# Kernel tuning notes

Hardware: AMD Instinct MI355X
Metric: run time of the kernel (lower is better)

Reference implementation:

```python
import jax, jax.numpy as jnp
import numpy as np

B, C1, H, W = 8, 256, 192, 192
P = 4              # effective patch size (even, <= H,W)
ROUTE_RATIO = 0.25
MIN_REGIONS = 1
HIDDEN = 128       # max(int(c1*0.5), 16)
ROUTE_HIDDEN = 64  # max(HIDDEN//2, 16)
EPS = 1e-5


def conv2d(x, w, groups=1, pad=0):
    return jax.lax.conv_general_dilated(
        x, w, (1, 1), [(pad, pad), (pad, pad)],
        dimension_numbers=("NCHW", "OIHW", "NCHW"),
        feature_group_count=groups)


def bn(x, g, b):
    # eval-mode BatchNorm with running_mean=0, running_var=1
    scale = g / jnp.sqrt(1.0 + EPS)
    return x * scale[None, :, None, None] + b[None, :, None, None]


def pixel_unshuffle(x, r):
    n, c, h, w = x.shape
    x = x.reshape(n, c, h // r, r, w // r, r)
    return x.transpose(0, 1, 3, 5, 2, 4).reshape(n, c * r * r, h // r, w // r)


def pixel_shuffle(x, r):
    n, cr, h, w = x.shape
    c = cr // (r * r)
    x = x.reshape(n, c, r, r, h, w)
    return x.transpose(0, 1, 4, 2, 5, 3).reshape(n, c, h * r, w * r)


def setup_inputs() -> dict:
    key = jax.random.key(0)
    ks = jax.random.split(key, 8)
    c4 = C1 * 4
    inp = {
        "x": jax.random.normal(ks[0], (B, C1, H, W), jnp.float32),
        # route head: 1x1 conv (no bias) -> BN -> SiLU -> 1x1 conv (bias)
        "rw1": jax.random.normal(ks[1], (ROUTE_HIDDEN, C1, 1, 1), jnp.float32) / np.sqrt(C1),
        "rg1": jnp.ones((ROUTE_HIDDEN,), jnp.float32),
        "rb1": jnp.zeros((ROUTE_HIDDEN,), jnp.float32),
        "rw2": jax.random.normal(ks[2], (1, ROUTE_HIDDEN, 1, 1), jnp.float32) / np.sqrt(ROUTE_HIDDEN),
        "rbias2": jnp.zeros((1,), jnp.float32),
        # expert: Conv(4c->hidden,1x1)+BN+SiLU, DWConv(3x3)+BN+SiLU, Conv(hidden->4c,1x1)+BN
        "ew1": jax.random.normal(ks[3], (HIDDEN, c4, 1, 1), jnp.float32) / np.sqrt(c4),
        "eg1": jnp.ones((HIDDEN,), jnp.float32),
        "eb1": jnp.zeros((HIDDEN,), jnp.float32),
        "dww": jax.random.normal(ks[4], (HIDDEN, 1, 3, 3), jnp.float32) / 3.0,
        "dwg": jnp.ones((HIDDEN,), jnp.float32),
        "dwb": jnp.zeros((HIDDEN,), jnp.float32),
        "ew2": jax.random.normal(ks[5], (c4, HIDDEN, 1, 1), jnp.float32) / np.sqrt(HIDDEN),
        "eg2": jnp.ones((c4,), jnp.float32),
        "eb2": jnp.zeros((c4,), jnp.float32),
    }
    return inp


def reference(x, rw1, rg1, rb1, rw2, rbias2, ew1, eg1, eb1, dww, dwg, dwb, ew2, eg2, eb2):
    b, c, h, w = x.shape
    p = P
    pad_h = (p - h % p) % p
    pad_w = (p - w % p) % p
    x_pad = jnp.pad(x, ((0, 0), (0, 0), (0, pad_h), (0, pad_w)))
    hp, wp = h + pad_h, w + pad_w
    gh, gw = hp // p, wp // p
    num_patches = gh * gw
    k = min(num_patches, max(MIN_REGIONS, int(np.ceil(num_patches * ROUTE_RATIO))))

    # router: avg-pool each patch, 1x1 MLP -> per-patch score
    pooled = x_pad.reshape(b, c, gh, p, gw, p).mean(axis=(3, 5))          # [b,c,gh,gw]
    r1 = jax.nn.silu(bn(conv2d(pooled, rw1), rg1, rb1))
    logits = conv2d(r1, rw2) + rbias2[None, :, None, None]
    scores = jax.nn.sigmoid(logits).reshape(b, num_patches)               # [b,N]
    top_vals, top_idx = jax.lax.top_k(scores, k)                          # [b,k]

    # gather selected patches
    patches = x_pad.reshape(b, c, gh, p, gw, p).transpose(0, 2, 4, 1, 3, 5)
    patches = patches.reshape(b, num_patches, c, p, p)
    sel = jnp.take_along_axis(patches, top_idx[:, :, None, None, None], axis=1)
    sel = sel.reshape(b * k, c, p, p)

    # expert on pixel-unshuffled patches
    y = pixel_unshuffle(sel, 2)                                           # [bk, 4c, p/2, p/2]
    y = jax.nn.silu(bn(conv2d(y, ew1), eg1, eb1))
    y = jax.nn.silu(bn(conv2d(y, dww, groups=HIDDEN, pad=1), dwg, dwb))
    y = bn(conv2d(y, ew2), eg2, eb2)
    refined = pixel_shuffle(y, 2).reshape(b, k, c, p, p)
    refined = refined * top_vals[:, :, None, None, None]

    # scatter back into zero residual
    delta = jnp.zeros((b, num_patches, c, p, p), x.dtype)
    delta = delta.at[jnp.arange(b)[:, None], top_idx].set(refined)
    delta = delta.reshape(b, gh, gw, c, p, p).transpose(0, 3, 1, 4, 2, 5)
    delta = delta.reshape(b, c, hp, wp)
    return delta[..., :h, :w]
```

## Files before the change

### kernel.cpp

```cpp
#include <hip/hip_runtime.h>
#include <hip/hip_bf16.h>

typedef __attribute__((ext_vector_type(8))) short bf16x8;
typedef __attribute__((ext_vector_type(4))) float f32x4;

#define NB 8
#define C1 256
#define HH 192
#define WW 192
#define GH 48
#define GW 48
#define NP 2304
#define KSEL 576
#define RH 64
#define HID 128
#define C4 1024
#define HW (HH*WW)

#define WS_FLAG 0
#define WS_F 64
#define WS_W16 81280ull
#define WS_POOLED 605696ull
#define WS_PSCALE WS_POOLED
#define WS_SCORES 19480064ull

#define F_RW1 0
#define F_RG1 16384
#define F_RB1 16448
#define F_RW2 16512
#define F_RBIAS2 16576
#define F_EG1 16580
#define F_EB1 16708
#define F_DWW 16836
#define F_DWG 17988
#define F_DWB 18116
#define F_EG2 18244
#define F_EB2 19268

__device__ __forceinline__ float b2f(unsigned short h) {
  return __uint_as_float(((unsigned)h) << 16);
}
__device__ __forceinline__ unsigned short f2b(float f) {
  unsigned u = __float_as_uint(f);
  u += 0x7FFF + ((u >> 16) & 1u);
  return (unsigned short)(u >> 16);
}
__device__ __forceinline__ float siluf(float v) { return v / (1.f + expf(-v)); }

__global__ void k_detect(const unsigned short* xb, char* ws) {
  __shared__ int cnt[256];
  int t = threadIdx.x;
  int c = 0;
  for (int s = 0; s < 32; ++s) {
    unsigned short u = xb[(t * 32 + s) * 2];
    int e = (u >> 7) & 0xFF;
    c += (u == 0 || (e >= 90 && e <= 145)) ? 1 : 0;
  }
  cnt[t] = c;
  __syncthreads();
  for (int s = 128; s > 0; s >>= 1) {
    if (t < s) cnt[t] += cnt[t + s];
    __syncthreads();
  }
  if (t == 0) *(int*)(ws + WS_FLAG) = (cnt[0] >= 4915) ? 1 : 0;
}

__global__ void k_prep(const void* rw1, const void* rg1, const void* rb1, const void* rw2,
                       const void* rbias2, const void* ew1, const void* eg1, const void* eb1,
                       const void* dww, const void* dwg, const void* dwb, const void* ew2,
                       const void* eg2, const void* eb2, char* ws) {
  int bf = *(const int*)(ws + WS_FLAG);
  float* F = (float*)(ws + WS_F);
  unsigned short* W16 = (unsigned short*)(ws + WS_W16);
  int i = blockIdx.x * 256 + threadIdx.x;
  if (i >= 282433) return;
  if (i < 20289) {
    const void* src; int si; int dof;
    if      (i < 16384) { src = rw1;    si = i;          dof = F_RW1 + si; }
    else if (i < 16448) { src = rg1;    si = i - 16384;  dof = F_RG1 + si; }
    else if (i < 16512) { src = rb1;    si = i - 16448;  dof = F_RB1 + si; }
    else if (i < 16576) { src = rw2;    si = i - 16512;  dof = F_RW2 + si; }
    else if (i < 16577) { src = rbias2; si = i - 16576;  dof = F_RBIAS2 + si; }
    else if (i < 16705) { src = eg1;    si = i - 16577;  dof = F_EG1 + si; }
    else if (i < 16833) { src = eb1;    si = i - 16705;  dof = F_EB1 + si; }
    else if (i < 17985) { src = dww;    si = i - 16833;  dof = F_DWW + si; }
    else if (i < 18113) { src = dwg;    si = i - 17985;  dof = F_DWG + si; }
    else if (i < 18241) { src = dwb;    si = i - 18113;  dof = F_DWB + si; }
    else if (i < 19265) { src = eg2;    si = i - 18241;  dof = F_EG2 + si; }
    else                { src = eb2;    si = i - 19265;  dof = F_EB2 + si; }
    F[dof] = bf ? b2f(((const unsigned short*)src)[si]) : ((const float*)src)[si];
  } else {
    int j = i - 20289;
    const void* src; int si; int dof;
    if (j < 131072) { src = ew1; si = j;          dof = j; }
    else            { src = ew2; si = j - 131072; dof = j; }
    W16[dof] = bf ? ((const unsigned short*)src)[si]
                  : f2b(((const float*)src)[si]);
  }
}

template<int BF>
__global__ void k_pool(const void* xin, char* ws) {
  if ((*(const int*)(ws + WS_FLAG) != 0) != (BF != 0)) return;
  float* pooled = (float*)(ws + WS_POOLED);
  int tid = blockIdx.x * 256 + threadIdx.x;
  int px = tid % GW;
  int t2 = tid / GW;
  int py = t2 % GH;
  int bc = t2 / GH;
  size_t base = (size_t)bc * HW + (size_t)(py * 4) * WW + px * 4;
  float s = 0.f;
#pragma unroll
  for (int r = 0; r < 4; ++r) {
    if (BF) {
      const ushort4 v = *(const ushort4*)((const unsigned short*)xin + base + r * WW);
      s += b2f(v.x) + b2f(v.y) + b2f(v.z) + b2f(v.w);
    } else {
      const float4 v = *(const float4*)((const float*)xin + base + r * WW);
      s += v.x + v.y + v.z + v.w;
    }
  }
  pooled[tid] = s * 0.0625f;
}

__global__ __launch_bounds__(512, 2) void k_mlp(char* ws) {
  const float* F = (const float*)(ws + WS_F);
  const float* pooled = (const float*)(ws + WS_POOLED);
  float* scores = (float*)(ws + WS_SCORES);
  __shared__ float LP[256][68];
  __shared__ float LR[8 * 64];
  const int t = threadIdx.x;
  const int b = blockIdx.x / 36;
  const int pos0 = (blockIdx.x % 36) * 64;

  {
    const int pc = t & 15, c0 = t >> 4;
    const float* src = pooled + (size_t)(b * C1) * NP + pos0 + pc * 4;
#pragma unroll
    for (int s = 0; s < 8; ++s) {
      int c = c0 + 32 * s;
      float4 v = *(const float4*)(src + (size_t)c * NP);
      *(float4*)&LP[c][pc * 4] = v;
    }
  }
  __syncthreads();

  const int lane = t & 63;
  const int q = __builtin_amdgcn_readfirstlane(t >> 6);
  const float* wq = F + F_RW1 + q * 8 * C1;
  float acc[8];
#pragma unroll
  for (int j = 0; j < 8; ++j) acc[j] = 0.f;
  for (int c = 0; c < 256; c += 4) {
    float p0 = LP[c + 0][lane];
    float p1 = LP[c + 1][lane];
    float p2 = LP[c + 2][lane];
    float p3 = LP[c + 3][lane];
#pragma unroll
    for (int j = 0; j < 8; ++j) {
      acc[j] += wq[j * C1 + c + 0] * p0;
      acc[j] += wq[j * C1 + c + 1] * p1;
      acc[j] += wq[j * C1 + c + 2] * p2;
      acc[j] += wq[j * C1 + c + 3] * p3;
    }
  }
  const float BNS = 1.f / sqrtf(1.f + 1e-5f);
  float lp = 0.f;
#pragma unroll
  for (int j = 0; j < 8; ++j) {
    int h = q * 8 + j;
    float v = acc[j] * (F[F_RG1 + h] * BNS) + F[F_RB1 + h];
    lp += F[F_RW2 + h] * siluf(v);
  }
  LR[q * 64 + lane] = lp;
  __syncthreads();
  if (t < 64) {
    float s = F[F_RBIAS2];
#pragma unroll
    for (int j = 0; j < 8; ++j) s += LR[j * 64 + t];
    scores[b * NP + pos0 + t] = 1.f / (1.f + expf(-s));
  }
}

__global__ void k_route(char* ws) {
  const float* scores = (const float*)(ws + WS_SCORES);
  float* pscale = (float*)(ws + WS_PSCALE);
  int b = blockIdx.x / 9, r = blockIdx.x % 9;
  __shared__ float s[NP];
  for (int i = threadIdx.x; i < NP; i += 256) s[i] = scores[b * NP + i];
  __syncthreads();
  int i = r * 256 + threadIdx.x;
  float si = s[i];
  int rank = 0;
  for (int j = 0; j < NP; ++j) {
    float sj = s[j];
    rank += (sj > si || (sj == si && j < i)) ? 1 : 0;
  }
  pscale[b * NP + i] = (rank < KSEL) ? si : 0.f;
}


#define XLOAD(P_, cc_) do { \
    size_t o_ = (size_t)(cc_) * 16 * HW; \
    if (BF) { P_##h0 = *(const ushort4*)(xh + xoff0 + o_); \
              P_##h1 = *(const ushort4*)(xh + xoff1 + o_); } \
    else    { P_##f0 = *(const float4*)(xf + xoff0 + o_); \
              P_##f1 = *(const float4*)(xf + xoff1 + o_); } \
    const unsigned short* wp_ = W1b + (cc_) * 64; \
    P_##w0 = *(const uint4*)(wp_ + wi0); \
    P_##w1 = *(const uint4*)(wp_ + wi1); \
  } while(0)

#define XWRITE(P_, UT_, WC_) do { \
    unsigned lo0_, hi0_, lo1_, hi1_; \
    if (BF) { lo0_ = P_##h0.x | ((unsigned)P_##h0.y << 16); hi0_ = P_##h0.z | ((unsigned)P_##h0.w << 16); \
              lo1_ = P_##h1.x | ((unsigned)P_##h1.y << 16); hi1_ = P_##h1.z | ((unsigned)P_##h1.w << 16); } \
    else    { lo0_ = f2b(P_##f0.x) | ((unsigned)f2b(P_##f0.y) << 16); hi0_ = f2b(P_##f0.z) | ((unsigned)f2b(P_##f0.w) << 16); \
              lo1_ = f2b(P_##f1.x) | ((unsigned)f2b(P_##f1.y) << 16); hi1_ = f2b(P_##f1.z) | ((unsigned)f2b(P_##f1.w) << 16); } \
    *(unsigned*)&UT_[n_lo72 + kb0] = lo0_; \
    *(unsigned*)&UT_[n_hi72 + kb0] = hi0_; \
    *(unsigned*)&UT_[n_lo72 + kb1] = lo1_; \
    *(unsigned*)&UT_[n_hi72 + kb1] = hi1_; \
    *(uint4*)&WC_[wcw0] = P_##w0; \
    *(uint4*)&WC_[wcw1] = P_##w1; \
  } while(0)

#define MFMA1(WCO_, B_, ACC_) ACC_ = __builtin_amdgcn_mfma_f32_16x16x32_bf16(*(const bf16x8*)&WC_[wc_off + (WCO_)], B_, ACC_, 0, 0, 0)

#define G1_MFMA(UT_, WCp_) do { \
    const unsigned short* WC_ = WCp_; \
    bf16x8 b0_ = *(const bf16x8*)&UT_[ut_off]; \
    bf16x8 b1_ = *(const bf16x8*)&UT_[ut_off + 32]; \
    MFMA1(0, b0_, acc10);    MFMA1(1152, b0_, acc11); \
    MFMA1(2304, b0_, acc12); MFMA1(3456, b0_, acc13); \
    MFMA1(32, b1_, acc10);   MFMA1(1152+32, b1_, acc11); \
    MFMA1(2304+32, b1_, acc12); MFMA1(3456+32, b1_, acc13); \
  } while(0)

#define G1EPI(ACC_, mi_) do { \
    _Pragma("unroll") \
    for (int r_ = 0; r_ < 4; ++r_) { \
      int h_ = 64 * wm + 16 * (mi_) + l4 * 4 + r_; \
      O1[h_ * 68 + otc] = siluf(ACC_[r_] * (F[F_EG1 + h_] * BNS) + F[F_EB1 + h_]); \
    } \
  } while(0)

#define G2_STEP(P_, WCp_, mt_) do { \
    const unsigned short* WC_ = WCp_; \
    *(uint4*)&((unsigned short*)WCp_)[w2a] = P_##a; \
    *(uint4*)&((unsigned short*)WCp_)[w2b] = P_##b; \
    if ((mt_) < 14) { \
      const unsigned short* wp_ = W2b + (size_t)((mt_) + 2) * 8192; \
      P_##a = *(const uint4*)(wp_ + w2s); \
      P_##b = *(const uint4*)(wp_ + w2s + 64); \
    } \
    __syncthreads(); \
    f32x4 a20 = (f32x4){0.f, 0.f, 0.f, 0.f}; \
    f32x4 a21 = (f32x4){0.f, 0.f, 0.f, 0.f}; \
    a20 = __builtin_amdgcn_mfma_f32_16x16x32_bf16(*(const bf16x8*)&WC_[g2_off + 0],        bq0, a20, 0,0,0); \
    a21 = __builtin_amdgcn_mfma_f32_16x16x32_bf16(*(const bf16x8*)&WC_[g2_off + 2176],     bq0, a21, 0,0,0); \
    a20 = __builtin_amdgcn_mfma_f32_16x16x32_bf16(*(const bf16x8*)&WC_[g2_off + 32],       bq1, a20, 0,0,0); \
    a21 = __builtin_amdgcn_mfma_f32_16x16x32_bf16(*(const bf16x8*)&WC_[g2_off + 2176+32],  bq1, a21, 0,0,0); \
    a20 = __builtin_amdgcn_mfma_f32_16x16x32_bf16(*(const bf16x8*)&WC_[g2_off + 64],       bq2, a20, 0,0,0); \
    a21 = __builtin_amdgcn_mfma_f32_16x16x32_bf16(*(const bf16x8*)&WC_[g2_off + 2176+64],  bq2, a21, 0,0,0); \
    a20 = __builtin_amdgcn_mfma_f32_16x16x32_bf16(*(const bf16x8*)&WC_[g2_off + 96],       bq3, a20, 0,0,0); \
    a21 = __builtin_amdgcn_mfma_f32_16x16x32_bf16(*(const bf16x8*)&WC_[g2_off + 2176+96],  bq3, a21, 0,0,0); \
    _Pragma("unroll") \
    for (int r_ = 0; r_ < 4; ++r_) { \
      int ml0_ = 32 * wm + l4 * 4 + r_; \
      int m20_ = (mt_) * 64 + ml0_; \
      OT[ml0_ * 68 + otc] = a20[r_] * (F[F_EG2 + m20_] * BNS) + F[F_EB2 + m20_]; \
      OT[(ml0_ + 16) * 68 + otc] = a21[r_] * (F[F_EG2 + m20_ + 16] * BNS) + F[F_EB2 + m20_ + 16]; \
    } \
    __syncthreads(); \
    _Pragma("unroll") \
    for (int s_ = 0; s_ < 2; ++s_) { \
      int cl_ = o_cl + 8 * s_; \
      int ch_ = (mt_) * 16 + cl_; \
      size_t ob_ = ((size_t)(bC1 + ch_) * HH + r0 + o_rr) * WW + c0 + o_p * 4; \
      int rb_ = (4 * cl_ + 2 * (o_rr & 1)) * 68 + (o_rr >> 1) * 32 + o_p; \
      float ps_ = PSs[o_p]; \
      float e0_ = OT[rb_] * ps_; \
      float e1_ = OT[rb_ + 68] * ps_; \
      float e2_ = OT[rb_ + 16] * ps_; \
      float e3_ = OT[rb_ + 68 + 16] * ps_; \
      if (BF) { ushort4 o4_ = {f2b(e0_), f2b(e1_), f2b(e2_), f2b(e3_)}; \
                *(ushort4*)((unsigned short*)outv + ob_) = o4_; } \
      else    { float4 o4_ = {e0_, e1_, e2_, e3_}; \
                *(float4*)((float*)outv + ob_) = o4_; } \
    } \
    __syncthreads(); \
  } while(0)

template<int BF>
__global__ __launch_bounds__(512, 4) void k_expert(const void* xin, void* outv, char* ws) {
  if ((*(const int*)(ws + WS_FLAG) != 0) != (BF != 0)) return;
  const float* F = (const float*)(ws + WS_F);
  const unsigned short* W1b = (const unsigned short*)(ws + WS_W16);
  const unsigned short* W2b = W1b + 131072;
  const float* pscale = (const float*)(ws + WS_PSCALE);

  __shared__ __align__(16) char LB[70720];
  unsigned short* UT0  = (unsigned short*)(LB);
  unsigned short* UT1  = (unsigned short*)(LB + 9216);
  unsigned short* WC0  = (unsigned short*)(LB + 18432);
  unsigned short* WC1  = (unsigned short*)(LB + 36864);
  float*          O1   = (float*)(LB + 18432);
  unsigned short* Y2T  = (unsigned short*)(LB);
  float*          OT   = (float*)(LB + 18432);
  unsigned short* WC20 = (unsigned short*)(LB + 35840);
  unsigned short* WC21 = (unsigned short*)(LB + 53248);
  float*          PSs  = (float*)(LB + 70656);

  const int t = threadIdx.x;
  const int lane = t & 63;
  const int w = t >> 6;
  const int wm = w >> 2, wn = w & 3;
  const int l15 = lane & 15, l4 = lane >> 4;
  const int bid = blockIdx.x;
  const int xq = bid % 3;
  const int py = (bid / 3) % GH;
  const int b  = bid / (3 * GH);
  const int r0 = py * 4, c0 = xq * 64;
  const int bC1 = b * C1;
  const float BNS = 1.f / sqrtf(1.f + 1e-5f);

  if (t < 16) PSs[t] = pscale[b * NP + py * GW + xq * 16 + t];

  const int rr = (t >> 4) & 3, v4 = t & 15;
  const int n_lo72 = (32 * (rr >> 1) + v4) * 72;
  const int n_hi72 = n_lo72 + 16 * 72;
  const int kb0 = 4 * w + 2 * (rr & 1);
  const int kb1 = kb0 + 32;
  const size_t xoff0 = ((size_t)bC1 + w) * HW + (size_t)(r0 + rr) * WW + c0 + v4 * 4;
  const size_t xoff1 = xoff0 + (size_t)8 * HW;
  const int m_0 = t >> 3, k8_0 = t & 7;
  const int wi0 = m_0 * 1024 + k8_0 * 8;
  const int wi1 = (m_0 + 64) * 1024 + k8_0 * 8;
  const int wcw0 = m_0 * 72 + k8_0 * 8;
  const int wcw1 = (m_0 + 64) * 72 + k8_0 * 8;
  const int ut_off = (16 * wn + l15) * 72 + l4 * 8;
  const int wc_off = (64 * wm + l15) * 72 + l4 * 8;
  const int otc = 16 * wn + l15;
  const int w2a = (t >> 3) * 136 + (t & 7) * 8;
  const int w2b = w2a + 64;
  const int w2s = (t >> 3) * 128 + (t & 7) * 8;
  const int g2_off = (32 * wm + l15) * 136 + l4 * 8;
  const int o_p = t & 15, o_rr = (t >> 4) & 3, o_cl = t >> 6;

  const float* xf = (const float*)xin;
  const unsigned short* xh = (const unsigned short*)xin;

  float4 Af0, Af1, Bf0, Bf1;
  ushort4 Ah0, Ah1, Bh0, Bh1;
  uint4 Aw0, Aw1, Bw0, Bw1;
  uint4 A2a, A2b, B2a, B2b;

  f32x4 acc10 = (f32x4){0.f,0.f,0.f,0.f};
  f32x4 acc11 = (f32x4){0.f,0.f,0.f,0.f};
  f32x4 acc12 = (f32x4){0.f,0.f,0.f,0.f};
  f32x4 acc13 = (f32x4){0.f,0.f,0.f,0.f};

  XLOAD(A, 0);
  XLOAD(B, 1);
  for (int cc2 = 0; cc2 < 8; ++cc2) {
    int cc = cc2 * 2;
    XWRITE(A, UT0, WC0);
    if (cc2 < 7) XLOAD(A, cc + 2);
    __syncthreads();
    G1_MFMA(UT0, WC0);
    XWRITE(B, UT1, WC1);
    if (cc2 < 7) XLOAD(B, cc + 3);
    __syncthreads();
    G1_MFMA(UT1, WC1);
  }

  A2a = *(const uint4*)(W2b + w2s);
  A2b = *(const uint4*)(W2b + w2s + 64);
  B2a = *(const uint4*)(W2b + 8192 + w2s);
  B2b = *(const uint4*)(W2b + 8192 + w2s + 64);

  __syncthreads();
  G1EPI(acc10, 0);
  G1EPI(acc11, 1);
  G1EPI(acc12, 2);
  G1EPI(acc13, 3);
  __syncthreads();

  {
    const int p = t & 15, hh = t >> 4;
#pragma unroll
    for (int s = 0; s < 4; ++s) {
      int h = hh + 32 * s;
      float i0 = O1[h * 68 + p];
      float i1 = O1[h * 68 + 16 + p];
      float i2 = O1[h * 68 + 32 + p];
      float i3 = O1[h * 68 + 48 + p];
      const float* kw = F + F_DWW + h * 9;
      float sd = F[F_DWG + h] * BNS, bd = F[F_DWB + h];
      float o00 = kw[4] * i0 + kw[5] * i1 + kw[7] * i2 + kw[8] * i3;
      float o01 = kw[3] * i0 + kw[4] * i1 + kw[6] * i2 + kw[7] * i3;
      float o10 = kw[1] * i0 + kw[2] * i1 + kw[4] * i2 + kw[5] * i3;
      float o11 = kw[0] * i0 + kw[1] * i1 + kw[3] * i2 + kw[4] * i3;
      Y2T[(0 * 16 + p) * 136 + h] = f2b(siluf(o00 * sd + bd));
      Y2T[(1 * 16 + p) * 136 + h] = f2b(siluf(o01 * sd + bd));
      Y2T[(2 * 16 + p) * 136 + h] = f2b(siluf(o10 * sd + bd));
      Y2T[(3 * 16 + p) * 136 + h] = f2b(siluf(o11 * sd + bd));
    }
  }
  __syncthreads();

  const int ybase = (16 * wn + l15) * 136 + l4 * 8;
  bf16x8 bq0 = *(const bf16x8*)&Y2T[ybase];
  bf16x8 bq1 = *(const bf16x8*)&Y2T[ybase + 32];
  bf16x8 bq2 = *(const bf16x8*)&Y2T[ybase + 64];
  bf16x8 bq3 = *(const bf16x8*)&Y2T[ybase + 96];

  for (int mtt = 0; mtt < 16; mtt += 2) {
    G2_STEP(A2, WC20, mtt);
    G2_STEP(B2, WC21, mtt + 1);
  }
}

extern "C" void kernel_launch(void* const* d_in, const int* in_sizes, int n_in,
                              void* d_out, int out_size, void* d_ws, size_t ws_size,
                              hipStream_t stream) {
  char* ws = (char*)d_ws;
  const void* x = d_in[0];
  k_detect<<<1, 256, 0, stream>>>((const unsigned short*)x, ws);
  k_prep<<<1104, 256, 0, stream>>>(d_in[1], d_in[2], d_in[3], d_in[4], d_in[5], d_in[6],
                                   d_in[7], d_in[8], d_in[9], d_in[10], d_in[11], d_in[12],
                                   d_in[13], d_in[14], ws);
  k_pool<1><<<18432, 256, 0, stream>>>(x, ws);
  k_pool<0><<<18432, 256, 0, stream>>>(x, ws);
  k_mlp<<<288, 512, 0, stream>>>(ws);
  k_route<<<72, 256, 0, stream>>>(ws);
  k_expert<1><<<1152, 512, 0, stream>>>(x, d_out, ws);
  k_expert<0><<<1152, 512, 0, stream>>>(x, d_out, ws);
}
```

Measured before the change: 329.3 us.

## Merge dtype-templated kernels into runtime-flag kernels and skip unselected patch loads

Replaces the paired bf16/fp32 template launches of the pooling and expert kernels with single launches that read the dtype flag at runtime, removing two launches that only returned early. The expert kernel now skips global x loads for patches whose route scale is zero and feeds zeros instead. It also uses a packed hardware fp32-to-bf16 convert instruction, and the dtype-detection probe now samples fewer, more widely strided elements. The risks are runtime branching inside the hot loop, possible extra register pressure from merging both paths into one kernel, and a detection heuristic that now relies on fewer samples.

```diff
diff --git a/kernel.cpp b/kernel.cpp
--- a/kernel.cpp
+++ b/kernel.cpp
@@ -51,8 +51,9 @@
   __shared__ int cnt[256];
   int t = threadIdx.x;
   int c = 0;
-  for (int s = 0; s < 32; ++s) {
-    unsigned short u = xb[(t * 32 + s) * 2];
+#pragma unroll
+  for (int s = 0; s < 8; ++s) {
+    unsigned short u = xb[(size_t)(t * 8 + s) * 1024];
     int e = (u >> 7) & 0xFF;
     c += (u == 0 || (e >= 90 && e <= 145)) ? 1 : 0;
   }
@@ -62,7 +63,7 @@
     if (t < s) cnt[t] += cnt[t + s];
     __syncthreads();
   }
-  if (t == 0) *(int*)(ws + WS_FLAG) = (cnt[0] >= 4915) ? 1 : 0;
+  if (t == 0) *(int*)(ws + WS_FLAG) = (cnt[0] >= 1229) ? 1 : 0;
 }
 
 __global__ void k_prep(const void* rw1, const void* rg1, const void* rb1, const void* rw2,
@@ -99,9 +100,8 @@
   }
 }
 
-template<int BF>
 __global__ void k_pool(const void* xin, char* ws) {
-  if ((*(const int*)(ws + WS_FLAG) != 0) != (BF != 0)) return;
+  const int bf = *(const int*)(ws + WS_FLAG);
   float* pooled = (float*)(ws + WS_POOLED);
   int tid = blockIdx.x * 256 + threadIdx.x;
   int px = tid % GW;
@@ -110,12 +110,15 @@
   int bc = t2 / GH;
   size_t base = (size_t)bc * HW + (size_t)(py * 4) * WW + px * 4;
   float s = 0.f;
-#pragma unroll
-  for (int r = 0; r < 4; ++r) {
-    if (BF) {
+  if (bf) {
+#pragma unroll
+    for (int r = 0; r < 4; ++r) {
       const ushort4 v = *(const ushort4*)((const unsigned short*)xin + base + r * WW);
       s += b2f(v.x) + b2f(v.y) + b2f(v.z) + b2f(v.w);
-    } else {
+    }
+  } else {
+#pragma unroll
+    for (int r = 0; r < 4; ++r) {
       const float4 v = *(const float4*)((const float*)xin + base + r * WW);
       s += v.x + v.y + v.z + v.w;
     }
@@ -201,11 +204,13 @@
 
 
 #define XLOAD(P_, cc_) do { \
-    size_t o_ = (size_t)(cc_) * 16 * HW; \
-    if (BF) { P_##h0 = *(const ushort4*)(xh + xoff0 + o_); \
-              P_##h1 = *(const ushort4*)(xh + xoff1 + o_); } \
-    else    { P_##f0 = *(const float4*)(xf + xoff0 + o_); \
-              P_##f1 = *(const float4*)(xf + xoff1 + o_); } \
+    if (sel) { \
+      size_t o_ = (size_t)(cc_) * 16 * HW; \
+      if (BF) { P_##h0 = *(const ushort4*)(xh + xoff0 + o_); \
+                P_##h1 = *(const ushort4*)(xh + xoff1 + o_); } \
+      else    { P_##f0 = *(const float4*)(xf + xoff0 + o_); \
+                P_##f1 = *(const float4*)(xf + xoff1 + o_); } \
+    } \
     const unsigned short* wp_ = W1b + (cc_) * 64; \
     P_##w0 = *(const uint4*)(wp_ + wi0); \
     P_##w1 = *(const uint4*)(wp_ + wi1); \
@@ -215,8 +220,10 @@
     unsigned lo0_, hi0_, lo1_, hi1_; \
     if (BF) { lo0_ = P_##h0.x | ((unsigned)P_##h0.y << 16); hi0_ = P_##h0.z | ((unsigned)P_##h0.w << 16); \
               lo1_ = P_##h1.x | ((unsigned)P_##h1.y << 16); hi1_ = P_##h1.z | ((unsigned)P_##h1.w << 16); } \
-    else    { lo0_ = f2b(P_##f0.x) | ((unsigned)f2b(P_##f0.y) << 16); hi0_ = f2b(P_##f0.z) | ((unsigned)f2b(P_##f0.w) << 16); \
-              lo1_ = f2b(P_##f1.x) | ((unsigned)f2b(P_##f1.y) << 16); hi1_ = f2b(P_##f1.z) | ((unsigned)f2b(P_##f1.w) << 16); } \
+    else    { asm("v_cvt_pk_bf16_f32 %0, %1, %2" : "=v"(lo0_) : "v"(P_##f0.x), "v"(P_##f0.y)); \
+              asm("v_cvt_pk_bf16_f32 %0, %1, %2" : "=v"(hi0_) : "v"(P_##f0.z), "v"(P_##f0.w)); \
+              asm("v_cvt_pk_bf16_f32 %0, %1, %2" : "=v"(lo1_) : "v"(P_##f1.x), "v"(P_##f1.y)); \
+              asm("v_cvt_pk_bf16_f32 %0, %1, %2" : "=v"(hi1_) : "v"(P_##f1.z), "v"(P_##f1.w)); } \
     *(unsigned*)&UT_[n_lo72 + kb0] = lo0_; \
     *(unsigned*)&UT_[n_hi72 + kb0] = hi0_; \
     *(unsigned*)&UT_[n_lo72 + kb1] = lo1_; \
@@ -292,9 +299,8 @@
     __syncthreads(); \
   } while(0)
 
-template<int BF>
 __global__ __launch_bounds__(512, 4) void k_expert(const void* xin, void* outv, char* ws) {
-  if ((*(const int*)(ws + WS_FLAG) != 0) != (BF != 0)) return;
+  const int BF = *(const int*)(ws + WS_FLAG);
   const float* F = (const float*)(ws + WS_F);
   const unsigned short* W1b = (const unsigned short*)(ws + WS_W16);
   const unsigned short* W2b = W1b + 131072;
@@ -326,6 +332,8 @@
   const float BNS = 1.f / sqrtf(1.f + 1e-5f);
 
   if (t < 16) PSs[t] = pscale[b * NP + py * GW + xq * 16 + t];
+  __syncthreads();
+  const bool sel = PSs[t & 15] != 0.f;
 
   const int rr = (t >> 4) & 3, v4 = t & 15;
   const int n_lo72 = (32 * (rr >> 1) + v4) * 72;
@@ -351,8 +359,8 @@
   const float* xf = (const float*)xin;
   const unsigned short* xh = (const unsigned short*)xin;
 
-  float4 Af0, Af1, Bf0, Bf1;
-  ushort4 Ah0, Ah1, Bh0, Bh1;
+  float4 Af0 = {0,0,0,0}, Af1 = {0,0,0,0}, Bf0 = {0,0,0,0}, Bf1 = {0,0,0,0};
+  ushort4 Ah0 = {0,0,0,0}, Ah1 = {0,0,0,0}, Bh0 = {0,0,0,0}, Bh1 = {0,0,0,0};
   uint4 Aw0, Aw1, Bw0, Bw1;
   uint4 A2a, A2b, B2a, B2b;
 
@@ -431,10 +439,8 @@
   k_prep<<<1104, 256, 0, stream>>>(d_in[1], d_in[2], d_in[3], d_in[4], d_in[5], d_in[6],
                                    d_in[7], d_in[8], d_in[9], d_in[10], d_in[11], d_in[12],
                                    d_in[13], d_in[14], ws);
-  k_pool<1><<<18432, 256, 0, stream>>>(x, ws);
-  k_pool<0><<<18432, 256, 0, stream>>>(x, ws);
+  k_pool<<<18432, 256, 0, stream>>>(x, ws);
   k_mlp<<<288, 512, 0, stream>>>(ws);
   k_route<<<72, 256, 0, stream>>>(ws);
-  k_expert<1><<<1152, 512, 0, stream>>>(x, d_out, ws);
-  k_expert<0><<<1152, 512, 0, stream>>>(x, d_out, ws);
-}
+  k_expert<<<1152, 512, 0, stream>>>(x, d_out, ws);
+}
```

Result: faster. 319.9 us (-2.9%).
